# Optimization experiments

Hardware: AMD Instinct MI355X
Metric: run time of the kernel (lower is better)

Reference implementation:

```python
import jax, jax.numpy as jnp
import numpy as np

N, D, H, C = 16384, 2048, 512, 65
EPS_LOG = 1e-6   # matches torch log(p + 1e-6)
EPS_NORM = 1e-12 # matches F.normalize default eps


def setup_inputs() -> dict:
    key = jax.random.key(0)
    k0, k1, k2 = jax.random.split(key, 3)
    return {
        "feat": jax.random.normal(k0, (N, D), jnp.float32),
        "w1": jax.random.normal(k1, (D, H), jnp.float32) * (1.0 / np.sqrt(D)),
        "b1": jnp.zeros((H,), jnp.float32),
        "w2": jax.random.normal(k2, (H, C), jnp.float32) * (1.0 / np.sqrt(H)),
        "b2": jnp.zeros((C,), jnp.float32),
    }


def reference(feat, w1, b1, w2, b2):
    n, c = feat.shape[0], w2.shape[1]
    # fc1 -> relu -> dropout(p=0.5, training=True; fixed key for determinism) -> fc2
    h = jax.nn.relu(feat @ w1 + b1)
    keep = jax.random.bernoulli(jax.random.key(42), 0.5, h.shape)
    h = jnp.where(keep, h * 2.0, 0.0)
    logits = h @ w2 + b2

    logp = jax.nn.log_softmax(logits, axis=1)
    p = jnp.exp(logp)  # softmax_out

    entropy = -jnp.mean(jnp.sum(p * jnp.log(p + EPS_LOG), axis=1))
    mean_p = jnp.mean(p, axis=0)
    diversity = jnp.sum(mean_p * jnp.log(mean_p + EPS_LOG))

    # per-class centroids: one-pass segment reduce instead of python loop over classes
    pseudo_preds = jnp.argmax(p, axis=1)
    sums = jax.ops.segment_sum(feat, pseudo_preds, num_segments=c)          # [C, D]
    counts = jax.ops.segment_sum(jnp.ones((n,), feat.dtype), pseudo_preds, num_segments=c)
    means = sums / jnp.maximum(counts, 1.0)[:, None]
    norms = jnp.linalg.norm(means, axis=1, keepdims=True)
    centroids = jnp.where(counts[:, None] > 0, means / jnp.maximum(norms, EPS_NORM), 0.0)

    feat_n = feat / jnp.maximum(jnp.linalg.norm(feat, axis=1, keepdims=True), EPS_NORM)
    sim = feat_n @ centroids.T                                              # [N, C]
    pseudo_labels = jnp.argmax(sim, axis=1)

    ce = -jnp.mean(jnp.take_along_axis(logp, pseudo_labels[:, None], axis=1))
    loss = entropy + diversity + 0.3 * ce
    return loss
```

## Files before the change

kernel.cpp:

```cpp
#include <hip/hip_runtime.h>

typedef unsigned short us;
typedef unsigned int u32;
typedef __attribute__((ext_vector_type(8))) short short8;
typedef __attribute__((ext_vector_type(4))) float f32x4;

#define MFMA16(a, b, c) __builtin_amdgcn_mfma_f32_16x16x32_bf16((a), (b), (c), 0, 0, 0)

#define GLD16(lptr, gptr) __builtin_amdgcn_global_load_lds( \
    (__attribute__((address_space(1))) void*)(gptr), \
    (__attribute__((address_space(3))) void*)(lptr), 16, 0, 0)

__device__ inline us f2bf(float f) {
  u32 u = __float_as_uint(f);
  u32 r = (u + 0x7FFFu + ((u >> 16) & 1u)) >> 16;
  return (us)r;
}
__device__ inline float bf2f(us s) { return __uint_as_float((u32)s << 16); }
__device__ inline void splitbf(float x, us& hi, us& lo) {
  hi = f2bf(x);
  lo = f2bf(x - bf2f(hi));
}

#define TF_R(a) { x0 += x1; x1 = (x1 << (a)) | (x1 >> (32 - (a))); x1 ^= x0; }
__global__ __launch_bounds__(256) void k_prep(
    const float* __restrict__ feat, const float* __restrict__ w1, const float* __restrict__ w2,
    us* __restrict__ xh, us* __restrict__ xl,
    us* __restrict__ w1h, us* __restrict__ w1l,
    us* __restrict__ w2h, us* __restrict__ w2l,
    u32* __restrict__ mask, float* __restrict__ accs,
    int* __restrict__ cnt, int* __restrict__ cursor, int* __restrict__ done) {
  __shared__ float tile[64][65];
  int b = blockIdx.x, t = threadIdx.x;
  if (b < 16384) {
    size_t g = ((size_t)b * 256 + t) * 8;
    f32x4 a = *(const f32x4*)(feat + g);
    f32x4 bb = *(const f32x4*)(feat + g + 4);
    short8 h8, l8;
    for (int i = 0; i < 4; ++i) {
      us hi, lo;
      splitbf(a[i], hi, lo); h8[i] = (short)hi; l8[i] = (short)lo;
      splitbf(bb[i], hi, lo); h8[4 + i] = (short)hi; l8[4 + i] = (short)lo;
    }
    *(short8*)(xh + g) = h8;
    *(short8*)(xl + g) = l8;
  } else if (b < 16896) {
    u32 tt = (u32)(b - 16384) * 256u + (u32)t;
    const u32 K0 = 0u, K1 = 42u, K2 = 0x1BD11BDAu ^ 0u ^ 42u;
    u32 w0 = 0, w1r = 0;
    for (int i = 0; i < 32; ++i) {
      u32 x0 = tt * 32u + (u32)i;
      u32 x1 = x0 + 4194304u;
      x0 += K0; x1 += K1;
      TF_R(13) TF_R(15) TF_R(26) TF_R(6)   x0 += K1; x1 += K2 + 1u;
      TF_R(17) TF_R(29) TF_R(16) TF_R(24)  x0 += K2; x1 += K0 + 2u;
      TF_R(13) TF_R(15) TF_R(26) TF_R(6)   x0 += K0; x1 += K1 + 3u;
      TF_R(17) TF_R(29) TF_R(16) TF_R(24)  x0 += K1; x1 += K2 + 4u;
      TF_R(13) TF_R(15) TF_R(26) TF_R(6)   x0 += K2; x1 += K0 + 5u;
      w0 |= (u32)((x0 >> 31) == 0u) << i;
      w1r |= (u32)((x1 >> 31) == 0u) << i;
    }
    mask[tt] = w0;
    mask[tt + 131072u] = w1r;
  } else if (b < 17152) {
    int i = b - 16896;
    int k0 = (i & 31) * 64, n0 = (i >> 5) * 64;
    int cr = t >> 6, cc = t & 63;
    for (int j = 0; j < 16; ++j) {
      int r = j * 4 + cr;
      tile[r][cc] = w1[(size_t)(k0 + r) * 512 + n0 + cc];
    }
    __syncthreads();
    for (int j = 0; j < 16; ++j) {
      int n = j * 4 + cr;
      int k = cc;
      us hi, lo; splitbf(tile[k][n], hi, lo);
      size_t o = (size_t)(n0 + n) * 2048 + k0 + k;
      w1h[o] = hi; w1l[o] = lo;
    }
  } else if (b < 17232) {
    int n = b - 17152;
    for (int k = t; k < 512; k += 256) {
      float v = (n < 65) ? w2[(size_t)k * 65 + n] : 0.f;
      us hi, lo; splitbf(v, hi, lo);
      w2h[n * 512 + k] = hi; w2l[n * 512 + k] = lo;
    }
  } else {
    if (t < 68) accs[t] = 0.f;
    if (t < 65) { cnt[t] = 0; cursor[t] = 0; }
    if (t == 0) done[0] = 0;
  }
}

__global__ __launch_bounds__(256, 2) void k_gemm1(
    const us* __restrict__ Ah_, const us* __restrict__ Al_,
    const us* __restrict__ Bh_, const us* __restrict__ Bl_,
    const float* __restrict__ b1, const u32* __restrict__ mask,
    const us* __restrict__ W2h_, const us* __restrict__ W2l_,
    float* __restrict__ logitsP ) {
  __shared__ __align__(16) us lds[4 * 8192];
  us* sAh = lds; us* sAl = lds + 8192; us* sBh = lds + 16384; us* sBl = lds + 24576;
  int tid = threadIdx.x;
  int bm = blockIdx.x, bn = blockIdx.y;
  int m0 = bm * 128, n0 = bn * 128;
  int lane = tid & 63, wv = tid >> 6;
  int wm = (wv >> 1) * 64, wn = (wv & 1) * 64;
  int frow = lane & 15, fq = lane >> 4;
  int quad = lane >> 4;
  int srow = tid >> 3;
  int scolsw = (((tid & 7) ^ ((tid >> 3) & 7)) * 8);
  f32x4 acc[4][4] = {};
  size_t arow = (size_t)(m0 + srow) * 2048 + scolsw;
  size_t brow = (size_t)(n0 + srow) * 2048 + scolsw;
  for (int kt = 0; kt < 32; ++kt) {
    int k0 = kt * 64;
    __syncthreads();
#pragma unroll
    for (int j = 0; j < 4; ++j) {
      int lo = j * 2048 + wv * 512;
      size_t go = (size_t)j * 32 * 2048 + k0;
      GLD16(sAh + lo, Ah_ + arow + go);
      GLD16(sAl + lo, Al_ + arow + go);
      GLD16(sBh + lo, Bh_ + brow + go);
      GLD16(sBl + lo, Bl_ + brow + go);
    }
    __syncthreads();
#pragma unroll
    for (int s = 0; s < 2; ++s) {
      short8 ah[4], al[4], bh[4], bl[4];
#pragma unroll
      for (int f = 0; f < 4; ++f) {
        int ca = ((s * 4 + fq) ^ (frow & 7)) * 8;
        int ra = (wm + f * 16 + frow) * 64 + ca;
        int rb = (wn + f * 16 + frow) * 64 + ca;
        ah[f] = *(const short8*)&sAh[ra];
        al[f] = *(const short8*)&sAl[ra];
        bh[f] = *(const short8*)&sBh[rb];
        bl[f] = *(const short8*)&sBl[rb];
      }
#pragma unroll
      for (int i = 0; i < 4; ++i)
#pragma unroll
        for (int j2 = 0; j2 < 4; ++j2) {
          acc[i][j2] = MFMA16(ah[i], bh[j2], acc[i][j2]);
          acc[i][j2] = MFMA16(ah[i], bl[j2], acc[i][j2]);
          acc[i][j2] = MFMA16(al[i], bh[j2], acc[i][j2]);
        }
    }
  }
  __syncthreads();
  us* sHh = lds;
  us* sHl = lds + 16384;
#pragma unroll
  for (int i = 0; i < 4; ++i)
#pragma unroll
    for (int j = 0; j < 4; ++j)
#pragma unroll
      for (int r = 0; r < 4; ++r) {
        int row = wm + i * 16 + quad * 4 + r;
        int colL = wn + j * 16 + (lane & 15);
        float v = acc[i][j][r] + b1[n0 + colL];
        v = fmaxf(v, 0.f);
        u32 f = (u32)(m0 + row) * 512u + (u32)(n0 + colL);
        u32 keep = (mask[f >> 5] >> (f & 31u)) & 1u;
        v = keep ? v * 2.f : 0.f;
        us hi, lo; splitbf(v, hi, lo);
        int slab = colL >> 6, k2 = colL & 63;
        int chunk = ((k2 >> 3) ^ (row & 7));
        int a = slab * 8192 + row * 64 + chunk * 8 + (k2 & 7);
        sHh[a] = hi; sHl[a] = lo;
      }
  __syncthreads();
  int wm2 = wv * 32;
  f32x4 accm[2][5] = {};
#pragma unroll
  for (int ks = 0; ks < 4; ++ks) {
    int slab = ks >> 1;
    short8 a_h[2], a_l[2];
#pragma unroll
    for (int mf = 0; mf < 2; ++mf) {
      int crow = wm2 + mf * 16 + frow;
      int cm = ((((ks & 1) * 4 + fq) ^ (frow & 7))) * 8;
      int a = slab * 8192 + crow * 64 + cm;
      a_h[mf] = *(const short8*)&sHh[a];
      a_l[mf] = *(const short8*)&sHl[a];
    }
#pragma unroll
    for (int fn = 0; fn < 5; ++fn) {
      int c = fn * 16 + frow;
      size_t bo = (size_t)c * 512 + n0 + ks * 32 + fq * 8;
      short8 b_h = *(const short8*)(W2h_ + bo);
      short8 b_l = *(const short8*)(W2l_ + bo);
#pragma unroll
      for (int mf = 0; mf < 2; ++mf) {
        accm[mf][fn] = MFMA16(a_h[mf], b_h, accm[mf][fn]);
        accm[mf][fn] = MFMA16(a_h[mf], b_l, accm[mf][fn]);
        accm[mf][fn] = MFMA16(a_l[mf], b_h, accm[mf][fn]);
      }
    }
  }
#pragma unroll
  for (int mf = 0; mf < 2; ++mf)
#pragma unroll
    for (int fn = 0; fn < 5; ++fn)
#pragma unroll
      for (int r = 0; r < 4; ++r) {
        int grow = m0 + wm2 + mf * 16 + quad * 4 + r;
        int c = fn * 16 + (lane & 15);
        logitsP[((size_t)bn * 16384 + grow) * 80 + c] = accm[mf][fn][r];
      }
}

__global__ __launch_bounds__(256) void k_softmax(
    const float* __restrict__ logitsP, const float* __restrict__ b2,
    float* __restrict__ logp, int* __restrict__ preds,
    float* __restrict__ accs , int* __restrict__ cnt) {
  __shared__ float slog[64 * 81];
  __shared__ float sm[64], sl[64];
  __shared__ float sred[256];
  __shared__ int hh[65];
  int tid = threadIdx.x;
  int m0 = blockIdx.x * 64;
  int r = tid >> 2, cg = tid & 3;
  const float* p0 = logitsP + (size_t)(m0 + r) * 80;
#pragma unroll
  for (int cc = 0; cc < 5; ++cc) {
    int c = cg * 20 + cc * 4;
    f32x4 v = *(const f32x4*)(p0 + c);
    v += *(const f32x4*)(p0 + 16384ull * 80 + c);
    v += *(const f32x4*)(p0 + 2ull * 16384 * 80 + c);
    v += *(const f32x4*)(p0 + 3ull * 16384 * 80 + c);
#pragma unroll
    for (int e = 0; e < 4; ++e) {
      int c2 = c + e;
      if (c2 < 65) slog[r * 81 + c2] = v[e] + b2[c2];
    }
  }
  if (tid < 65) hh[tid] = 0;
  __syncthreads();
  if (tid < 64) {
    int row = tid;
    float m = -1e30f; int am = 0;
    for (int c = 0; c < 65; ++c) {
      float v = slog[row * 81 + c];
      if (v > m) { m = v; am = c; }
    }
    float s = 0.f;
    for (int c = 0; c < 65; ++c) s += expf(slog[row * 81 + c] - m);
    sm[row] = m; sl[row] = logf(s);
    preds[m0 + row] = am;
    atomicAdd(&hh[am], 1);
  }
  __syncthreads();
  if (tid < 65 && hh[tid] > 0) atomicAdd(&cnt[tid], hh[tid]);
  float entp = 0.f;
  if (tid < 240) {
    int c = tid % 80, rr0 = tid / 80;
    if (c < 65) {
      float mpp = 0.f;
      for (int rr = rr0; rr < 64; rr += 3) {
        float v = slog[rr * 81 + c] - sm[rr] - sl[rr];
        logp[(size_t)(m0 + rr) * 65 + c] = v;
        float p = expf(v);
        mpp += p;
        entp += p * logf(p + 1e-6f);
      }
      atomicAdd(&accs[2 + c], mpp);
    }
  }
  sred[tid] = entp;
  __syncthreads();
  for (int s = 128; s > 0; s >>= 1) { if (tid < s) sred[tid] += sred[tid + s]; __syncthreads(); }
  if (tid == 0) atomicAdd(&accs[0], sred[0]);
}

__global__ __launch_bounds__(256) void k_scatter(
    const int* __restrict__ preds, const int* __restrict__ cnt,
    int* __restrict__ cursor, int* __restrict__ rowidx) {
  __shared__ int h[65];
  __shared__ int gb[65];
  __shared__ int sbase[65];
  int tid = threadIdx.x;
  if (tid < 65) { h[tid] = 0; sbase[tid] = cnt[tid]; }
  __syncthreads();
  int i = blockIdx.x * 256 + tid;
  int c = preds[i];
  int pos = atomicAdd(&h[c], 1);
  if (tid == 0) {
    int s = 0;
    for (int cc = 0; cc < 65; ++cc) { int v = sbase[cc]; sbase[cc] = s; s += v; }
  }
  __syncthreads();
  if (tid < 65 && h[tid] > 0) gb[tid] = atomicAdd(&cursor[tid], h[tid]);
  __syncthreads();
  rowidx[sbase[c] + gb[c] + pos] = i;
}

__global__ __launch_bounds__(256) void k_segsum2(
    const float* __restrict__ feat, const int* __restrict__ rowidx,
    const int* __restrict__ cnt,
    float* __restrict__ psum ) {
  int c = blockIdx.x;
  int j = blockIdx.y;
  int tid = threadIdx.x;
  int start = 0;
  for (int cc = 0; cc < 65; ++cc) { if (cc == c) break; start += cnt[cc]; }
  int n = cnt[c];
  f32x4 a0 = {}, a1 = {};
  const float* fp = feat + (size_t)tid * 8;
  for (int i = j; i < n; i += 16) {
    int row = rowidx[start + i];
    const f32x4* p = (const f32x4*)(fp + (size_t)row * 2048);
    a0 += p[0];
    a1 += p[1];
  }
  float* o = psum + ((size_t)(j * 65 + c)) * 2048 + (size_t)tid * 8;
  *(f32x4*)o = a0;
  *(f32x4*)(o + 4) = a1;
}

__global__ __launch_bounds__(256) void k_centroid(
    const float* __restrict__ psum, const int* __restrict__ pcnt,
    us* __restrict__ ch, us* __restrict__ cl) {
  int c = blockIdx.x;
  int tid = threadIdx.x;
  if (c >= 65) {
    for (int d = tid; d < 2048; d += 256) { ch[(size_t)c * 2048 + d] = 0; cl[(size_t)c * 2048 + d] = 0; }
    return;
  }
  int cnt = pcnt[c];
  float inv = 1.0f / (float)((cnt > 1) ? cnt : 1);
  float mean[8]; float sq = 0.f;
  for (int i = 0; i < 8; ++i) {
    int d = tid + i * 256;
    float s = 0.f;
    for (int nc = 0; nc < 16; ++nc) s += psum[((size_t)nc * 65 + c) * 2048 + d];
    mean[i] = s * inv;
    sq += mean[i] * mean[i];
  }
  __shared__ float red[256];
  red[tid] = sq; __syncthreads();
  for (int s = 128; s > 0; s >>= 1) { if (tid < s) red[tid] += red[tid + s]; __syncthreads(); }
  float norm = sqrtf(red[0]);
  float dscale = (cnt > 0) ? 1.0f / fmaxf(norm, 1e-12f) : 0.0f;
  for (int i = 0; i < 8; ++i) {
    int d = tid + i * 256;
    us hi, lo; splitbf(mean[i] * dscale, hi, lo);
    ch[(size_t)c * 2048 + d] = hi; cl[(size_t)c * 2048 + d] = lo;
  }
}

__global__ __launch_bounds__(256, 2) void k_sim(
    const us* __restrict__ Ah_, const us* __restrict__ Al_,
    const us* __restrict__ Bh_, const us* __restrict__ Bl_,
    float* __restrict__ simbuf ) {
  __shared__ __align__(16) us sA[2][4096];
  __shared__ __align__(16) us sB[2][5120];
  int tid = threadIdx.x;
  int m0 = blockIdx.x * 64;
  int ks = blockIdx.y;
  int kbase = ks * 512;
  int lane = tid & 63, wv = tid >> 6;
  int frow = lane & 15, fq = lane >> 4;
  int srow = tid >> 3;
  int scolsw = (((tid & 7) ^ ((tid >> 3) & 7)) * 8);
  f32x4 acc[5] = {};
  size_t arow = (size_t)(m0 + srow) * 2048 + kbase + scolsw;
  size_t brow = (size_t)srow * 2048 + kbase + scolsw;
  size_t brow2 = (size_t)(64 + (tid >> 3)) * 2048 + kbase + scolsw;
  for (int kt = 0; kt < 8; ++kt) {
    int k0 = kt * 64;
    __syncthreads();
#pragma unroll
    for (int j = 0; j < 2; ++j) {
      int lo = j * 2048 + wv * 512;
      size_t go = (size_t)j * 32 * 2048 + k0;
      GLD16(&sA[0][lo], Ah_ + arow + go);
      GLD16(&sA[1][lo], Al_ + arow + go);
      GLD16(&sB[0][lo], Bh_ + brow + go);
      GLD16(&sB[1][lo], Bl_ + brow + go);
    }
    if (wv < 2) {
      GLD16(&sB[0][4096 + wv * 512], Bh_ + brow2 + k0);
      GLD16(&sB[1][4096 + wv * 512], Bl_ + brow2 + k0);
    }
    __syncthreads();
#pragma unroll
    for (int s = 0; s < 2; ++s) {
      int ca = ((s * 4 + fq) ^ (frow & 7)) * 8;
      short8 a_h = *(const short8*)&sA[0][(wv * 16 + frow) * 64 + ca];
      short8 a_l = *(const short8*)&sA[1][(wv * 16 + frow) * 64 + ca];
#pragma unroll
      for (int fn = 0; fn < 5; ++fn) {
        short8 b_h = *(const short8*)&sB[0][(fn * 16 + frow) * 64 + ca];
        short8 b_l = *(const short8*)&sB[1][(fn * 16 + frow) * 64 + ca];
        acc[fn] = MFMA16(a_h, b_h, acc[fn]);
        acc[fn] = MFMA16(a_h, b_l, acc[fn]);
        acc[fn] = MFMA16(a_l, b_h, acc[fn]);
      }
    }
  }
#pragma unroll
  for (int fn = 0; fn < 5; ++fn) {
    int col = fn * 16 + (lane & 15);
#pragma unroll
    for (int r = 0; r < 4; ++r) {
      int row = wv * 16 + (lane >> 4) * 4 + r;
      simbuf[((size_t)(ks * 16384 + m0 + row)) * 80 + col] = acc[fn][r];
    }
  }
}

__global__ __launch_bounds__(256) void k_simred(
    const float* __restrict__ simbuf, const float* __restrict__ logp,
    float* __restrict__ accs, int* __restrict__ done, float* __restrict__ out) {
  __shared__ float sred[256];
  __shared__ int lastflag;
  int tid = threadIdx.x;
  int row = blockIdx.x * 256 + tid;
  const float* p0 = simbuf + (size_t)row * 80;
  float m = -1e30f; int am = 0;
  for (int c = 0; c < 65; ++c) {
    float v = p0[c] + p0[16384ull * 80 + c] + p0[2ull * 16384 * 80 + c] + p0[3ull * 16384 * 80 + c];
    if (v > m) { m = v; am = c; }
  }
  sred[tid] = logp[(size_t)row * 65 + am];
  __syncthreads();
  for (int s = 128; s > 0; s >>= 1) { if (tid < s) sred[tid] += sred[tid + s]; __syncthreads(); }
  if (tid == 0) {
    atomicAdd(&accs[1], sred[0]);
    __threadfence();
    int old = atomicAdd(done, 1);
    lastflag = (old == 63);
  }
  __syncthreads();
  if (!lastflag) return;
  float d = 0.f;
  if (tid < 65) {
    float mp = atomicAdd(&accs[2 + tid], 0.f) * (1.f / 16384.f);
    d = mp * logf(mp + 1e-6f);
  }
  sred[tid] = d;
  __syncthreads();
  for (int s = 128; s > 0; s >>= 1) { if (tid < s) sred[tid] += sred[tid + s]; __syncthreads(); }
  if (tid == 0) {
    float entropy = -atomicAdd(&accs[0], 0.f) * (1.f / 16384.f);
    float ce = -atomicAdd(&accs[1], 0.f) * (1.f / 16384.f);
    out[0] = entropy + sred[0] + 0.3f * ce;
  }
}

extern "C" void kernel_launch(void* const* d_in, const int* in_sizes, int n_in,
                              void* d_out, int out_size, void* d_ws, size_t ws_size,
                              hipStream_t stream) {
  const float* feat = (const float*)d_in[0];
  const float* w1   = (const float*)d_in[1];
  const float* b1   = (const float*)d_in[2];
  const float* w2   = (const float*)d_in[3];
  const float* b2   = (const float*)d_in[4];
  float* out = (float*)d_out;

  char* w = (char*)d_ws;
  auto alloc = [&](size_t b) { char* p = w; w += (b + 255) & ~(size_t)255; return p; };
  us*  feat_hi = (us*)alloc(16384ull * 2048 * 2);
  us*  feat_lo = (us*)alloc(16384ull * 2048 * 2);
  us*  w1t_hi  = (us*)alloc(512ull * 2048 * 2);
  us*  w1t_lo  = (us*)alloc(512ull * 2048 * 2);
  us*  w2t_hi  = (us*)alloc(80ull * 512 * 2);
  us*  w2t_lo  = (us*)alloc(80ull * 512 * 2);
  u32* mask    = (u32*)alloc(262144ull * 4);
  float* logitsP = (float*)alloc(4ull * 16384 * 80 * 4);
  float* logp  = (float*)alloc(16384ull * 65 * 4);
  int*   preds = (int*)alloc(16384ull * 4);
  float* psum  = (float*)alloc(16ull * 65 * 2048 * 4);
  int*   cnt   = (int*)alloc(65ull * 4);
  int*   cursor= (int*)alloc(65ull * 4);
  int*   rowidx= (int*)alloc(16384ull * 4);
  us*  cent_hi = (us*)alloc(80ull * 2048 * 2);
  us*  cent_lo = (us*)alloc(80ull * 2048 * 2);
  float* simbuf= (float*)alloc(4ull * 16384 * 80 * 4);
  float* accs  = (float*)alloc(68ull * 4);
  int*   done  = (int*)alloc(4ull);

  k_prep<<<17233, 256, 0, stream>>>(feat, w1, w2, feat_hi, feat_lo,
                                    w1t_hi, w1t_lo, w2t_hi, w2t_lo,
                                    mask, accs, cnt, cursor, done);
  k_gemm1<<<dim3(128, 4), 256, 0, stream>>>(feat_hi, feat_lo, w1t_hi, w1t_lo, b1, mask,
                                            w2t_hi, w2t_lo, logitsP);
  k_softmax<<<256, 256, 0, stream>>>(logitsP, b2, logp, preds, accs, cnt);
  k_scatter<<<64, 256, 0, stream>>>(preds, cnt, cursor, rowidx);
  k_segsum2<<<dim3(65, 16), 256, 0, stream>>>(feat, rowidx, cnt, psum);
  k_centroid<<<80, 256, 0, stream>>>(psum, cnt, cent_hi, cent_lo);
  k_sim<<<dim3(256, 4), 256, 0, stream>>>(feat_hi, feat_lo, cent_hi, cent_lo, simbuf);
  k_simred<<<64, 256, 0, stream>>>(simbuf, logp, accs, done, out);
}
```

Baseline: 478.6 us.

## Fuse post-GEMM stages into one persistent kernel with grid barriers

Replaces six small kernels (softmax, scatter, segment sum, centroid, similarity GEMM, reduction) with one 256-block persistent kernel that separates the phases with software grid barriers built on atomics. The similarity GEMM now runs the full K range per block instead of splitting K four ways, so the argmax is done in shared memory and the partial simbuf round trip through global memory goes away. The goal is to cut launch gaps and that extra traffic. In exchange, the similarity stage has only 256 blocks doing serial K work, and the barrier relies on all 256 blocks being co-resident, which risks deadlock if occupancy allows fewer.

```diff
diff --git a/kernel.cpp b/kernel.cpp
--- a/kernel.cpp
+++ b/kernel.cpp
@@ -29,7 +29,8 @@
     us* __restrict__ w1h, us* __restrict__ w1l,
     us* __restrict__ w2h, us* __restrict__ w2l,
     u32* __restrict__ mask, float* __restrict__ accs,
-    int* __restrict__ cnt, int* __restrict__ cursor, int* __restrict__ done) {
+    int* __restrict__ cnt, int* __restrict__ cursor, int* __restrict__ done,
+    int* __restrict__ bar) {
   __shared__ float tile[64][65];
   int b = blockIdx.x, t = threadIdx.x;
   if (b < 16384) {
@@ -88,6 +89,7 @@
   } else {
     if (t < 68) accs[t] = 0.f;
     if (t < 65) { cnt[t] = 0; cursor[t] = 0; }
+    if (t < 8) bar[t] = 0;
     if (t == 0) done[0] = 0;
   }
 }
@@ -211,242 +213,254 @@
       }
 }
 
-__global__ __launch_bounds__(256) void k_softmax(
-    const float* __restrict__ logitsP, const float* __restrict__ b2,
+__device__ inline void gridbar(int* bar, int idx) {
+  __syncthreads();
+  if (threadIdx.x == 0) {
+    __threadfence();
+    atomicAdd(&bar[idx], 1);
+    while (atomicAdd(&bar[idx], 0) < 256) __builtin_amdgcn_s_sleep(2);
+  }
+  __syncthreads();
+  __threadfence();
+}
+
+__global__ __launch_bounds__(256, 2) void k_post(
+    const float* __restrict__ feat, const float* __restrict__ b2,
+    const float* __restrict__ logitsP,
+    const us* __restrict__ Ah_, const us* __restrict__ Al_,
     float* __restrict__ logp, int* __restrict__ preds,
-    float* __restrict__ accs , int* __restrict__ cnt) {
-  __shared__ float slog[64 * 81];
-  __shared__ float sm[64], sl[64];
-  __shared__ float sred[256];
-  __shared__ int hh[65];
+    float* __restrict__ accs, int* __restrict__ cnt, int* __restrict__ cursor,
+    int* __restrict__ rowidx, float* __restrict__ psum ,
+    us* __restrict__ ch, us* __restrict__ cl,
+    int* __restrict__ bar, int* __restrict__ done, float* __restrict__ out) {
+  __shared__ __align__(16) char smem[58880];
   int tid = threadIdx.x;
-  int m0 = blockIdx.x * 64;
-  int r = tid >> 2, cg = tid & 3;
-  const float* p0 = logitsP + (size_t)(m0 + r) * 80;
-#pragma unroll
-  for (int cc = 0; cc < 5; ++cc) {
-    int c = cg * 20 + cc * 4;
-    f32x4 v = *(const f32x4*)(p0 + c);
-    v += *(const f32x4*)(p0 + 16384ull * 80 + c);
-    v += *(const f32x4*)(p0 + 2ull * 16384 * 80 + c);
-    v += *(const f32x4*)(p0 + 3ull * 16384 * 80 + c);
-#pragma unroll
-    for (int e = 0; e < 4; ++e) {
-      int c2 = c + e;
-      if (c2 < 65) slog[r * 81 + c2] = v[e] + b2[c2];
-    }
-  }
-  if (tid < 65) hh[tid] = 0;
-  __syncthreads();
-  if (tid < 64) {
-    int row = tid;
-    float m = -1e30f; int am = 0;
-    for (int c = 0; c < 65; ++c) {
-      float v = slog[row * 81 + c];
-      if (v > m) { m = v; am = c; }
-    }
-    float s = 0.f;
-    for (int c = 0; c < 65; ++c) s += expf(slog[row * 81 + c] - m);
-    sm[row] = m; sl[row] = logf(s);
-    preds[m0 + row] = am;
-    atomicAdd(&hh[am], 1);
-  }
-  __syncthreads();
-  if (tid < 65 && hh[tid] > 0) atomicAdd(&cnt[tid], hh[tid]);
-  float entp = 0.f;
-  if (tid < 240) {
-    int c = tid % 80, rr0 = tid / 80;
-    if (c < 65) {
-      float mpp = 0.f;
-      for (int rr = rr0; rr < 64; rr += 3) {
-        float v = slog[rr * 81 + c] - sm[rr] - sl[rr];
-        logp[(size_t)(m0 + rr) * 65 + c] = v;
-        float p = expf(v);
-        mpp += p;
-        entp += p * logf(p + 1e-6f);
-      }
-      atomicAdd(&accs[2 + c], mpp);
-    }
-  }
-  sred[tid] = entp;
-  __syncthreads();
-  for (int s = 128; s > 0; s >>= 1) { if (tid < s) sred[tid] += sred[tid + s]; __syncthreads(); }
-  if (tid == 0) atomicAdd(&accs[0], sred[0]);
-}
-
-__global__ __launch_bounds__(256) void k_scatter(
-    const int* __restrict__ preds, const int* __restrict__ cnt,
-    int* __restrict__ cursor, int* __restrict__ rowidx) {
-  __shared__ int h[65];
-  __shared__ int gb[65];
-  __shared__ int sbase[65];
-  int tid = threadIdx.x;
-  if (tid < 65) { h[tid] = 0; sbase[tid] = cnt[tid]; }
-  __syncthreads();
-  int i = blockIdx.x * 256 + tid;
-  int c = preds[i];
-  int pos = atomicAdd(&h[c], 1);
-  if (tid == 0) {
-    int s = 0;
-    for (int cc = 0; cc < 65; ++cc) { int v = sbase[cc]; sbase[cc] = s; s += v; }
-  }
-  __syncthreads();
-  if (tid < 65 && h[tid] > 0) gb[tid] = atomicAdd(&cursor[tid], h[tid]);
-  __syncthreads();
-  rowidx[sbase[c] + gb[c] + pos] = i;
-}
-
-__global__ __launch_bounds__(256) void k_segsum2(
-    const float* __restrict__ feat, const int* __restrict__ rowidx,
-    const int* __restrict__ cnt,
-    float* __restrict__ psum ) {
-  int c = blockIdx.x;
-  int j = blockIdx.y;
-  int tid = threadIdx.x;
-  int start = 0;
-  for (int cc = 0; cc < 65; ++cc) { if (cc == c) break; start += cnt[cc]; }
-  int n = cnt[c];
-  f32x4 a0 = {}, a1 = {};
-  const float* fp = feat + (size_t)tid * 8;
-  for (int i = j; i < n; i += 16) {
-    int row = rowidx[start + i];
-    const f32x4* p = (const f32x4*)(fp + (size_t)row * 2048);
-    a0 += p[0];
-    a1 += p[1];
-  }
-  float* o = psum + ((size_t)(j * 65 + c)) * 2048 + (size_t)tid * 8;
-  *(f32x4*)o = a0;
-  *(f32x4*)(o + 4) = a1;
-}
-
-__global__ __launch_bounds__(256) void k_centroid(
-    const float* __restrict__ psum, const int* __restrict__ pcnt,
-    us* __restrict__ ch, us* __restrict__ cl) {
-  int c = blockIdx.x;
-  int tid = threadIdx.x;
-  if (c >= 65) {
-    for (int d = tid; d < 2048; d += 256) { ch[(size_t)c * 2048 + d] = 0; cl[(size_t)c * 2048 + d] = 0; }
-    return;
-  }
-  int cnt = pcnt[c];
-  float inv = 1.0f / (float)((cnt > 1) ? cnt : 1);
-  float mean[8]; float sq = 0.f;
-  for (int i = 0; i < 8; ++i) {
-    int d = tid + i * 256;
-    float s = 0.f;
-    for (int nc = 0; nc < 16; ++nc) s += psum[((size_t)nc * 65 + c) * 2048 + d];
-    mean[i] = s * inv;
-    sq += mean[i] * mean[i];
-  }
-  __shared__ float red[256];
-  red[tid] = sq; __syncthreads();
-  for (int s = 128; s > 0; s >>= 1) { if (tid < s) red[tid] += red[tid + s]; __syncthreads(); }
-  float norm = sqrtf(red[0]);
-  float dscale = (cnt > 0) ? 1.0f / fmaxf(norm, 1e-12f) : 0.0f;
-  for (int i = 0; i < 8; ++i) {
-    int d = tid + i * 256;
-    us hi, lo; splitbf(mean[i] * dscale, hi, lo);
-    ch[(size_t)c * 2048 + d] = hi; cl[(size_t)c * 2048 + d] = lo;
-  }
-}
-
-__global__ __launch_bounds__(256, 2) void k_sim(
-    const us* __restrict__ Ah_, const us* __restrict__ Al_,
-    const us* __restrict__ Bh_, const us* __restrict__ Bl_,
-    float* __restrict__ simbuf ) {
-  __shared__ __align__(16) us sA[2][4096];
-  __shared__ __align__(16) us sB[2][5120];
-  int tid = threadIdx.x;
-  int m0 = blockIdx.x * 64;
-  int ks = blockIdx.y;
-  int kbase = ks * 512;
-  int lane = tid & 63, wv = tid >> 6;
-  int frow = lane & 15, fq = lane >> 4;
-  int srow = tid >> 3;
-  int scolsw = (((tid & 7) ^ ((tid >> 3) & 7)) * 8);
-  f32x4 acc[5] = {};
-  size_t arow = (size_t)(m0 + srow) * 2048 + kbase + scolsw;
-  size_t brow = (size_t)srow * 2048 + kbase + scolsw;
-  size_t brow2 = (size_t)(64 + (tid >> 3)) * 2048 + kbase + scolsw;
-  for (int kt = 0; kt < 8; ++kt) {
-    int k0 = kt * 64;
-    __syncthreads();
-#pragma unroll
-    for (int j = 0; j < 2; ++j) {
-      int lo = j * 2048 + wv * 512;
-      size_t go = (size_t)j * 32 * 2048 + k0;
-      GLD16(&sA[0][lo], Ah_ + arow + go);
-      GLD16(&sA[1][lo], Al_ + arow + go);
-      GLD16(&sB[0][lo], Bh_ + brow + go);
-      GLD16(&sB[1][lo], Bl_ + brow + go);
-    }
-    if (wv < 2) {
-      GLD16(&sB[0][4096 + wv * 512], Bh_ + brow2 + k0);
-      GLD16(&sB[1][4096 + wv * 512], Bl_ + brow2 + k0);
-    }
-    __syncthreads();
-#pragma unroll
-    for (int s = 0; s < 2; ++s) {
-      int ca = ((s * 4 + fq) ^ (frow & 7)) * 8;
-      short8 a_h = *(const short8*)&sA[0][(wv * 16 + frow) * 64 + ca];
-      short8 a_l = *(const short8*)&sA[1][(wv * 16 + frow) * 64 + ca];
-#pragma unroll
-      for (int fn = 0; fn < 5; ++fn) {
-        short8 b_h = *(const short8*)&sB[0][(fn * 16 + frow) * 64 + ca];
-        short8 b_l = *(const short8*)&sB[1][(fn * 16 + frow) * 64 + ca];
-        acc[fn] = MFMA16(a_h, b_h, acc[fn]);
-        acc[fn] = MFMA16(a_h, b_l, acc[fn]);
-        acc[fn] = MFMA16(a_l, b_h, acc[fn]);
-      }
-    }
-  }
-#pragma unroll
-  for (int fn = 0; fn < 5; ++fn) {
-    int col = fn * 16 + (lane & 15);
-#pragma unroll
-    for (int r = 0; r < 4; ++r) {
-      int row = wv * 16 + (lane >> 4) * 4 + r;
-      simbuf[((size_t)(ks * 16384 + m0 + row)) * 80 + col] = acc[fn][r];
-    }
-  }
-}
-
-__global__ __launch_bounds__(256) void k_simred(
-    const float* __restrict__ simbuf, const float* __restrict__ logp,
-    float* __restrict__ accs, int* __restrict__ done, float* __restrict__ out) {
-  __shared__ float sred[256];
-  __shared__ int lastflag;
-  int tid = threadIdx.x;
-  int row = blockIdx.x * 256 + tid;
-  const float* p0 = simbuf + (size_t)row * 80;
-  float m = -1e30f; int am = 0;
-  for (int c = 0; c < 65; ++c) {
-    float v = p0[c] + p0[16384ull * 80 + c] + p0[2ull * 16384 * 80 + c] + p0[3ull * 16384 * 80 + c];
-    if (v > m) { m = v; am = c; }
-  }
-  sred[tid] = logp[(size_t)row * 65 + am];
-  __syncthreads();
-  for (int s = 128; s > 0; s >>= 1) { if (tid < s) sred[tid] += sred[tid + s]; __syncthreads(); }
-  if (tid == 0) {
-    atomicAdd(&accs[1], sred[0]);
-    __threadfence();
-    int old = atomicAdd(done, 1);
-    lastflag = (old == 63);
-  }
-  __syncthreads();
-  if (!lastflag) return;
-  float d = 0.f;
-  if (tid < 65) {
-    float mp = atomicAdd(&accs[2 + tid], 0.f) * (1.f / 16384.f);
-    d = mp * logf(mp + 1e-6f);
-  }
-  sred[tid] = d;
-  __syncthreads();
-  for (int s = 128; s > 0; s >>= 1) { if (tid < s) sred[tid] += sred[tid + s]; __syncthreads(); }
-  if (tid == 0) {
-    float entropy = -atomicAdd(&accs[0], 0.f) * (1.f / 16384.f);
-    float ce = -atomicAdd(&accs[1], 0.f) * (1.f / 16384.f);
-    out[0] = entropy + sred[0] + 0.3f * ce;
+  int b = blockIdx.x;
+
+  {
+    float* slog = (float*)smem;
+    float* sm = (float*)(smem + 20736);
+    float* sl = (float*)(smem + 20992);
+    float* sred = (float*)(smem + 21248);
+    int* hh = (int*)(smem + 22272);
+    int m0 = b * 64;
+    int r = tid >> 2, cg = tid & 3;
+    const float* p0 = logitsP + (size_t)(m0 + r) * 80;
+#pragma unroll
+    for (int cc = 0; cc < 5; ++cc) {
+      int c = cg * 20 + cc * 4;
+      f32x4 v = *(const f32x4*)(p0 + c);
+      v += *(const f32x4*)(p0 + 16384ull * 80 + c);
+      v += *(const f32x4*)(p0 + 2ull * 16384 * 80 + c);
+      v += *(const f32x4*)(p0 + 3ull * 16384 * 80 + c);
+#pragma unroll
+      for (int e = 0; e < 4; ++e) {
+        int c2 = c + e;
+        if (c2 < 65) slog[r * 81 + c2] = v[e] + b2[c2];
+      }
+    }
+    if (tid < 65) hh[tid] = 0;
+    __syncthreads();
+    if (tid < 64) {
+      int row = tid;
+      float m = -1e30f; int am = 0;
+      for (int c = 0; c < 65; ++c) {
+        float v = slog[row * 81 + c];
+        if (v > m) { m = v; am = c; }
+      }
+      float s = 0.f;
+      for (int c = 0; c < 65; ++c) s += expf(slog[row * 81 + c] - m);
+      sm[row] = m; sl[row] = logf(s);
+      preds[m0 + row] = am;
+      atomicAdd(&hh[am], 1);
+    }
+    __syncthreads();
+    if (tid < 65 && hh[tid] > 0) atomicAdd(&cnt[tid], hh[tid]);
+    float entp = 0.f;
+    if (tid < 240) {
+      int c = tid % 80, rr0 = tid / 80;
+      if (c < 65) {
+        float mpp = 0.f;
+        for (int rr = rr0; rr < 64; rr += 3) {
+          float v = slog[rr * 81 + c] - sm[rr] - sl[rr];
+          logp[(size_t)(m0 + rr) * 65 + c] = v;
+          float p = expf(v);
+          mpp += p;
+          entp += p * logf(p + 1e-6f);
+        }
+        atomicAdd(&accs[2 + c], mpp);
+      }
+    }
+    sred[tid] = entp;
+    __syncthreads();
+    for (int s = 128; s > 0; s >>= 1) { if (tid < s) sred[tid] += sred[tid + s]; __syncthreads(); }
+    if (tid == 0) atomicAdd(&accs[0], sred[0]);
+  }
+  gridbar(bar, 0);
+
+  if (b < 64) {
+    int* h = (int*)smem;
+    int* gb = (int*)(smem + 272);
+    int* sbase = (int*)(smem + 544);
+    if (tid < 65) { h[tid] = 0; sbase[tid] = cnt[tid]; }
+    __syncthreads();
+    int i = b * 256 + tid;
+    int c = preds[i];
+    int pos = atomicAdd(&h[c], 1);
+    if (tid == 0) {
+      int s = 0;
+      for (int cc = 0; cc < 65; ++cc) { int v = sbase[cc]; sbase[cc] = s; s += v; }
+    }
+    __syncthreads();
+    if (tid < 65 && h[tid] > 0) gb[tid] = atomicAdd(&cursor[tid], h[tid]);
+    __syncthreads();
+    rowidx[sbase[c] + gb[c] + pos] = i;
+  }
+  gridbar(bar, 1);
+
+  {
+    for (int v = b; v < 65 * 16; v += 256) {
+      int c = v % 65, j = v / 65;
+      int start = 0;
+      for (int cc = 0; cc < c; ++cc) start += cnt[cc];
+      int n = cnt[c];
+      f32x4 a0 = {}, a1 = {};
+      const float* fp = feat + (size_t)tid * 8;
+      for (int i = j; i < n; i += 16) {
+        int row = rowidx[start + i];
+        const f32x4* p = (const f32x4*)(fp + (size_t)row * 2048);
+        a0 += p[0];
+        a1 += p[1];
+      }
+      float* o = psum + ((size_t)(j * 65 + c)) * 2048 + (size_t)tid * 8;
+      *(f32x4*)o = a0;
+      *(f32x4*)(o + 4) = a1;
+    }
+  }
+  gridbar(bar, 2);
+
+  if (b < 80) {
+    float* red = (float*)smem;
+    int c = b;
+    if (c >= 65) {
+      for (int d = tid; d < 2048; d += 256) { ch[(size_t)c * 2048 + d] = 0; cl[(size_t)c * 2048 + d] = 0; }
+    } else {
+      int cc = cnt[c];
+      float inv = 1.0f / (float)((cc > 1) ? cc : 1);
+      float mean[8]; float sq = 0.f;
+      for (int i = 0; i < 8; ++i) {
+        int d = tid + i * 256;
+        float s = 0.f;
+        for (int nc = 0; nc < 16; ++nc) s += psum[((size_t)nc * 65 + c) * 2048 + d];
+        mean[i] = s * inv;
+        sq += mean[i] * mean[i];
+      }
+      red[tid] = sq; __syncthreads();
+      for (int s = 128; s > 0; s >>= 1) { if (tid < s) red[tid] += red[tid + s]; __syncthreads(); }
+      float norm = sqrtf(red[0]);
+      float dscale = (cc > 0) ? 1.0f / fmaxf(norm, 1e-12f) : 0.0f;
+      for (int i = 0; i < 8; ++i) {
+        int d = tid + i * 256;
+        us hi, lo; splitbf(mean[i] * dscale, hi, lo);
+        ch[(size_t)c * 2048 + d] = hi; cl[(size_t)c * 2048 + d] = lo;
+      }
+    }
+  }
+  gridbar(bar, 3);
+
+  {
+    float* ssim = (float*)smem;
+    us* sA0 = (us*)(smem + 20736);
+    us* sA1 = (us*)(smem + 28928);
+    us* sB0 = (us*)(smem + 37120);
+    us* sB1 = (us*)(smem + 47360);
+    float* sred = (float*)(smem + 57600);
+    int m0 = b * 64;
+    int lane = tid & 63, wv = tid >> 6;
+    int frow = lane & 15, fq = lane >> 4;
+    int srow = tid >> 3;
+    int scolsw = (((tid & 7) ^ ((tid >> 3) & 7)) * 8);
+    f32x4 acc[5] = {};
+    size_t arow = (size_t)(m0 + srow) * 2048 + scolsw;
+    size_t brow = (size_t)srow * 2048 + scolsw;
+    size_t brow2 = (size_t)(64 + (tid >> 3)) * 2048 + scolsw;
+    for (int kt = 0; kt < 32; ++kt) {
+      int k0 = kt * 64;
+      __syncthreads();
+#pragma unroll
+      for (int j = 0; j < 2; ++j) {
+        int lo = j * 2048 + wv * 512;
+        size_t go = (size_t)j * 32 * 2048 + k0;
+        GLD16(sA0 + lo, Ah_ + arow + go);
+        GLD16(sA1 + lo, Al_ + arow + go);
+        GLD16(sB0 + lo, ((const us*)ch) + brow + go);
+        GLD16(sB1 + lo, ((const us*)cl) + brow + go);
+      }
+      if (wv < 2) {
+        GLD16(sB0 + 4096 + wv * 512, ((const us*)ch) + brow2 + k0);
+        GLD16(sB1 + 4096 + wv * 512, ((const us*)cl) + brow2 + k0);
+      }
+      __syncthreads();
+#pragma unroll
+      for (int s = 0; s < 2; ++s) {
+        int ca = ((s * 4 + fq) ^ (frow & 7)) * 8;
+        short8 a_h = *(const short8*)&sA0[(wv * 16 + frow) * 64 + ca];
+        short8 a_l = *(const short8*)&sA1[(wv * 16 + frow) * 64 + ca];
+#pragma unroll
+        for (int fn = 0; fn < 5; ++fn) {
+          short8 b_h = *(const short8*)&sB0[(fn * 16 + frow) * 64 + ca];
+          short8 b_l = *(const short8*)&sB1[(fn * 16 + frow) * 64 + ca];
+          acc[fn] = MFMA16(a_h, b_h, acc[fn]);
+          acc[fn] = MFMA16(a_h, b_l, acc[fn]);
+          acc[fn] = MFMA16(a_l, b_h, acc[fn]);
+        }
+      }
+    }
+    __syncthreads();
+#pragma unroll
+    for (int fn = 0; fn < 5; ++fn) {
+      int col = fn * 16 + (lane & 15);
+#pragma unroll
+      for (int r = 0; r < 4; ++r) {
+        int row = wv * 16 + (lane >> 4) * 4 + r;
+        ssim[row * 81 + col] = acc[fn][r];
+      }
+    }
+    __syncthreads();
+    float cep = 0.f;
+    if (tid < 64) {
+      float m = -1e30f; int am = 0;
+      for (int c = 0; c < 65; ++c) {
+        float v = ssim[tid * 81 + c];
+        if (v > m) { m = v; am = c; }
+      }
+      cep = logp[(size_t)(m0 + tid) * 65 + am];
+    }
+    sred[tid] = cep;
+    __syncthreads();
+    for (int s = 128; s > 0; s >>= 1) { if (tid < s) sred[tid] += sred[tid + s]; __syncthreads(); }
+    __shared__ int lastflag;
+    if (tid == 0) {
+      atomicAdd(&accs[1], sred[0]);
+      __threadfence();
+      int old = atomicAdd(done, 1);
+      lastflag = (old == 255);
+    }
+    __syncthreads();
+    if (!lastflag) return;
+    float d = 0.f;
+    if (tid < 65) {
+      float mp = atomicAdd(&accs[2 + tid], 0.f) * (1.f / 16384.f);
+      d = mp * logf(mp + 1e-6f);
+    }
+    sred[tid] = d;
+    __syncthreads();
+    for (int s = 128; s > 0; s >>= 1) { if (tid < s) sred[tid] += sred[tid + s]; __syncthreads(); }
+    if (tid == 0) {
+      float entropy = -atomicAdd(&accs[0], 0.f) * (1.f / 16384.f);
+      float ce = -atomicAdd(&accs[1], 0.f) * (1.f / 16384.f);
+      out[0] = entropy + sred[0] + 0.3f * ce;
+    }
   }
 }
 
@@ -478,19 +492,16 @@
   int*   rowidx= (int*)alloc(16384ull * 4);
   us*  cent_hi = (us*)alloc(80ull * 2048 * 2);
   us*  cent_lo = (us*)alloc(80ull * 2048 * 2);
-  float* simbuf= (float*)alloc(4ull * 16384 * 80 * 4);
   float* accs  = (float*)alloc(68ull * 4);
   int*   done  = (int*)alloc(4ull);
+  int*   bar   = (int*)alloc(32ull);
 
   k_prep<<<17233, 256, 0, stream>>>(feat, w1, w2, feat_hi, feat_lo,
                                     w1t_hi, w1t_lo, w2t_hi, w2t_lo,
-                                    mask, accs, cnt, cursor, done);
+                                    mask, accs, cnt, cursor, done, bar);
   k_gemm1<<<dim3(128, 4), 256, 0, stream>>>(feat_hi, feat_lo, w1t_hi, w1t_lo, b1, mask,
                                             w2t_hi, w2t_lo, logitsP);
-  k_softmax<<<256, 256, 0, stream>>>(logitsP, b2, logp, preds, accs, cnt);
-  k_scatter<<<64, 256, 0, stream>>>(preds, cnt, cursor, rowidx);
-  k_segsum2<<<dim3(65, 16), 256, 0, stream>>>(feat, rowidx, cnt, psum);
-  k_centroid<<<80, 256, 0, stream>>>(psum, cnt, cent_hi, cent_lo);
-  k_sim<<<dim3(256, 4), 256, 0, stream>>>(feat_hi, feat_lo, cent_hi, cent_lo, simbuf);
-  k_simred<<<64, 256, 0, stream>>>(simbuf, logp, accs, done, out);
-}
+  k_post<<<256, 256, 0, stream>>>(feat, b2, logitsP, feat_hi, feat_lo,
+                                  logp, preds, accs, cnt, cursor, rowidx, psum,
+                                  cent_hi, cent_lo, bar, done, out);
+}
```

Result: slower. 609.2 us (+27.3%).
